# Kernel optimization log

Measured on AMD Instinct MI355X. Metric: run time of the kernel, lower is better.

Reference implementation:

```python
import jax, jax.numpy as jnp
import numpy as np

NUM_HEADS = 24
HEAD_DIM = 128
DIM = NUM_HEADS * HEAD_DIM  # 3072
EPS = 1e-6


def rms_norm(x, g):
    # x: [b, h, s, d], g: [d]
    var = jnp.mean(jnp.square(x.astype(jnp.float32)), axis=-1, keepdims=True)
    return (x.astype(jnp.float32) * jax.lax.rsqrt(var + EPS)).astype(x.dtype) * g


def apply_rope(x, cos, sin):
    # x: [b, h, s, d]; cos/sin: [s, d//2]; complex multiply on interleaved pairs
    b, h, s, d = x.shape
    xr = x.reshape(b, h, s, d // 2, 2)
    x0, x1 = xr[..., 0], xr[..., 1]
    c = cos[None, None, :, :]
    sn = sin[None, None, :, :]
    o0 = x0 * c - x1 * sn
    o1 = x0 * sn + x1 * c
    return jnp.stack([o0, o1], axis=-1).reshape(b, h, s, d)


def split_heads(x):
    # [b, s, h*d] -> [b, h, s, d]
    b, s, _ = x.shape
    return x.reshape(b, s, NUM_HEADS, HEAD_DIM).transpose(0, 2, 1, 3)


def setup_inputs() -> dict:
    key = jax.random.key(0)
    ks = jax.random.split(key, 16)
    b, s_img, s_txt = 1, 2048, 256
    image = jax.random.normal(ks[0], (b, s_img, DIM), jnp.float32)
    text = jax.random.normal(ks[1], (b, s_txt, DIM), jnp.float32)
    # rotary freqs: angles = pos * inv_freq
    half = HEAD_DIM // 2
    inv_freq = 1.0 / (10000.0 ** (np.arange(half, dtype=np.float32) / half))
    ang_i = np.arange(s_img, dtype=np.float32)[:, None] * inv_freq[None, :]
    ang_t = np.arange(s_txt, dtype=np.float32)[:, None] * inv_freq[None, :]
    img_cos, img_sin = jnp.cos(jnp.asarray(ang_i)), jnp.sin(jnp.asarray(ang_i))
    txt_cos, txt_sin = jnp.cos(jnp.asarray(ang_t)), jnp.sin(jnp.asarray(ang_t))
    sc = 1.0 / np.sqrt(DIM)
    Wqkv = jax.random.normal(ks[2], (DIM, 3 * DIM), jnp.float32) * sc
    bqkv = jnp.zeros((3 * DIM,), jnp.float32)
    Wadd = jax.random.normal(ks[3], (DIM, 3 * DIM), jnp.float32) * sc
    badd = jnp.zeros((3 * DIM,), jnp.float32)
    gq = jnp.ones((HEAD_DIM,), jnp.float32)
    gk = jnp.ones((HEAD_DIM,), jnp.float32)
    gaq = jnp.ones((HEAD_DIM,), jnp.float32)
    gak = jnp.ones((HEAD_DIM,), jnp.float32)
    Wout = jax.random.normal(ks[4], (DIM, DIM), jnp.float32) * sc
    bout = jnp.zeros((DIM,), jnp.float32)
    Waddout = jax.random.normal(ks[5], (DIM, DIM), jnp.float32) * sc
    baddout = jnp.zeros((DIM,), jnp.float32)
    return dict(image=image, text=text, img_cos=img_cos, img_sin=img_sin,
                txt_cos=txt_cos, txt_sin=txt_sin, Wqkv=Wqkv, bqkv=bqkv,
                Wadd=Wadd, badd=badd, gq=gq, gk=gk, gaq=gaq, gak=gak,
                Wout=Wout, bout=bout, Waddout=Waddout, baddout=baddout)


def reference(image, text, img_cos, img_sin, txt_cos, txt_sin,
              Wqkv, bqkv, Wadd, badd, gq, gk, gaq, gak,
              Wout, bout, Waddout, baddout):
    seq_txt = text.shape[1]
    img_qkv = image @ Wqkv + bqkv
    img_q, img_k, img_v = jnp.split(img_qkv, 3, axis=-1)
    txt_qkv = text @ Wadd + badd
    txt_q, txt_k, txt_v = jnp.split(txt_qkv, 3, axis=-1)

    img_q, img_k, img_v = split_heads(img_q), split_heads(img_k), split_heads(img_v)
    txt_q, txt_k, txt_v = split_heads(txt_q), split_heads(txt_k), split_heads(txt_v)

    img_q, img_k = rms_norm(img_q, gq), rms_norm(img_k, gk)
    txt_q, txt_k = rms_norm(txt_q, gaq), rms_norm(txt_k, gak)

    img_q = apply_rope(img_q, img_cos, img_sin)
    img_k = apply_rope(img_k, img_cos, img_sin)
    txt_q = apply_rope(txt_q, txt_cos, txt_sin)
    txt_k = apply_rope(txt_k, txt_cos, txt_sin)

    # joint attention: text tokens first, then image tokens
    q = jnp.concatenate([txt_q, img_q], axis=2)  # [b, h, S, d]
    k = jnp.concatenate([txt_k, img_k], axis=2)
    v = jnp.concatenate([txt_v, img_v], axis=2)

    scale = 1.0 / np.sqrt(HEAD_DIM)
    scores = jnp.einsum('bhqd,bhkd->bhqk', q, k) * scale
    probs = jax.nn.softmax(scores, axis=-1)
    attn = jnp.einsum('bhqk,bhkd->bhqd', probs, v)
    b, h, S, d = attn.shape
    attn = attn.transpose(0, 2, 1, 3).reshape(b, S, h * d)  # [b, S, dim]

    txt_out = attn[:, :seq_txt, :]
    img_out = attn[:, seq_txt:, :]
    img_out = img_out @ Wout + bout
    txt_out = txt_out @ Waddout + baddout
    return img_out, txt_out
```

## Files before the change

kernel.cpp:

```cpp
#include <hip/hip_runtime.h>

#define NH 24
#define HD 128
#define DM 3072
#define DM3 9216
#define STXT 256
#define SIMG 2048
#define SALL 2304

typedef __attribute__((ext_vector_type(8))) short bfrag;
typedef __attribute__((ext_vector_type(4))) float ffrag;

__device__ __forceinline__ unsigned short f2bf(float f) {
  unsigned int x = __builtin_bit_cast(unsigned int, f);
  x += 0x7fffu + ((x >> 16) & 1u);
  return (unsigned short)(x >> 16);
}

__global__ __launch_bounds__(256) void cast_kernel(const float* __restrict__ in,
                                                   unsigned short* __restrict__ out) {
  int i = blockIdx.x * 256 + threadIdx.x;
  float4 a = ((const float4*)in)[2 * i];
  float4 b = ((const float4*)in)[2 * i + 1];
  uint4 o;
  o.x = (unsigned)f2bf(a.x) | ((unsigned)f2bf(a.y) << 16);
  o.y = (unsigned)f2bf(a.z) | ((unsigned)f2bf(a.w) << 16);
  o.z = (unsigned)f2bf(b.x) | ((unsigned)f2bf(b.y) << 16);
  o.w = (unsigned)f2bf(b.z) | ((unsigned)f2bf(b.w) << 16);
  ((uint4*)out)[i] = o;
}

__global__ __launch_bounds__(256) void transpose_cast_kernel(const float* __restrict__ W,
                                                             unsigned short* __restrict__ Wt,
                                                             int K, int N) {
  __shared__ __align__(16) unsigned short tile[64 * 72];
  int k0 = blockIdx.y * 64, n0 = blockIdx.x * 64;
  int t = threadIdx.x;
  int rr = t >> 4, cc = (t & 15) * 4;
#pragma unroll
  for (int p = 0; p < 4; ++p) {
    int k = rr + p * 16;
    float4 v = *(const float4*)&W[(size_t)(k0 + k) * N + n0 + cc];
    tile[(cc + 0) * 72 + k] = f2bf(v.x);
    tile[(cc + 1) * 72 + k] = f2bf(v.y);
    tile[(cc + 2) * 72 + k] = f2bf(v.z);
    tile[(cc + 3) * 72 + k] = f2bf(v.w);
  }
  __syncthreads();
  int n = t >> 2, c = (t & 3) * 16;
  float4* dst = (float4*)&Wt[(size_t)(n0 + n) * K + k0 + c];
  dst[0] = *(float4*)&tile[n * 72 + c];
  dst[1] = *(float4*)&tile[n * 72 + c + 8];
}

__global__ __launch_bounds__(256) void gemm_bt(const unsigned short* __restrict__ A,
                                               const unsigned short* __restrict__ Bt,
                                               const float* __restrict__ bias,
                                               int M, int N, int K, int mode,
                                               float* __restrict__ outf,
                                               unsigned short* __restrict__ outb, int s_off) {
  __shared__ __align__(16) unsigned short As[128 * 40];
  __shared__ __align__(16) unsigned short Bs[128 * 40];
  const int tid = threadIdx.x;
  const int wave = tid >> 6, lane = tid & 63, quad = lane >> 4, l16 = lane & 15;
  const int wm = (wave >> 1) * 64, wn = (wave & 1) * 64;
  const size_t m0 = (size_t)blockIdx.y * 128, n0 = (size_t)blockIdx.x * 128;

  ffrag zf = {0.f, 0.f, 0.f, 0.f};
  ffrag acc[4][4];
#pragma unroll
  for (int i = 0; i < 4; ++i)
#pragma unroll
    for (int j = 0; j < 4; ++j) acc[i][j] = zf;

  const int sr = tid >> 2;
  const int sc = (tid & 3) * 8;
  const unsigned short* Ag = A + (m0 + sr) * K + sc;
  const unsigned short* Bg = Bt + (n0 + sr) * K + sc;

  for (int k0 = 0; k0 < K; k0 += 32) {
    __syncthreads();
    *(bfrag*)&As[sr * 40 + sc] = *(const bfrag*)&Ag[k0];
    *(bfrag*)&As[(sr + 64) * 40 + sc] = *(const bfrag*)&Ag[(size_t)64 * K + k0];
    *(bfrag*)&Bs[sr * 40 + sc] = *(const bfrag*)&Bg[k0];
    *(bfrag*)&Bs[(sr + 64) * 40 + sc] = *(const bfrag*)&Bg[(size_t)64 * K + k0];
    __syncthreads();
    bfrag af[4], bfv[4];
#pragma unroll
    for (int mt = 0; mt < 4; ++mt)
      af[mt] = *(const bfrag*)&As[(wm + mt * 16 + l16) * 40 + quad * 8];
#pragma unroll
    for (int nt = 0; nt < 4; ++nt)
      bfv[nt] = *(const bfrag*)&Bs[(wn + nt * 16 + l16) * 40 + quad * 8];
#pragma unroll
    for (int mt = 0; mt < 4; ++mt)
#pragma unroll
      for (int nt = 0; nt < 4; ++nt)
        acc[mt][nt] = __builtin_amdgcn_mfma_f32_16x16x32_bf16(af[mt], bfv[nt], acc[mt][nt], 0, 0, 0);
  }

  float bv[4];
#pragma unroll
  for (int nt = 0; nt < 4; ++nt) bv[nt] = bias[n0 + wn + nt * 16 + l16];

#pragma unroll
  for (int mt = 0; mt < 4; ++mt) {
#pragma unroll
    for (int nt = 0; nt < 4; ++nt) {
      int gn = (int)n0 + wn + nt * 16 + l16;
#pragma unroll
      for (int r = 0; r < 4; ++r) {
        float v = acc[mt][nt][r] + bv[nt];
        int gm = (int)m0 + wm + mt * 16 + quad * 4 + r;
        if (mode == 2) {
          outf[(size_t)gm * N + gn] = v;
        } else {
          int which = gn / DM;
          int rr2 = gn - which * DM;
          int head = rr2 >> 7, d = rr2 & 127;
          int s = s_off + gm;
          if (which < 2)
            outf[(((size_t)which * NH + head) * SALL + s) * HD + d] = v;
          else
            outb[((size_t)head * HD + d) * SALL + s] = f2bf(v);
        }
      }
    }
  }
}

__global__ __launch_bounds__(256) void norm_rope_kernel(
    const float* __restrict__ qkvf, const float* __restrict__ gq, const float* __restrict__ gk,
    const float* __restrict__ gaq, const float* __restrict__ gak,
    const float* __restrict__ img_cos, const float* __restrict__ img_sin,
    const float* __restrict__ txt_cos, const float* __restrict__ txt_sin,
    unsigned short* __restrict__ Qb, unsigned short* __restrict__ Kb) {
  int wave = threadIdx.x >> 6, lane = threadIdx.x & 63;
  int row = blockIdx.x * 4 + wave;
  int which = row / (NH * SALL);
  int rem = row - which * (NH * SALL);
  int s = rem % SALL;
  float2 v = *(const float2*)&qkvf[(size_t)row * HD + lane * 2];
  float ss = v.x * v.x + v.y * v.y;
#pragma unroll
  for (int m = 1; m < 64; m <<= 1) ss += __shfl_xor(ss, m);
  float rinv = rsqrtf(ss * (1.0f / 128.0f) + 1e-6f);
  bool is_txt = s < STXT;
  int pos = is_txt ? s : s - STXT;
  const float* g = (which == 0) ? (is_txt ? gaq : gq) : (is_txt ? gak : gk);
  const float* ct = is_txt ? txt_cos : img_cos;
  const float* st = is_txt ? txt_sin : img_sin;
  float c = ct[pos * 64 + lane], sn = st[pos * 64 + lane];
  float x0 = v.x * rinv * g[lane * 2];
  float x1 = v.y * rinv * g[lane * 2 + 1];
  float o0 = x0 * c - x1 * sn;
  float o1 = x0 * sn + x1 * c;
  unsigned short* out = (which == 0 ? Qb : Kb) + (size_t)rem * HD + lane * 2;
  *(unsigned int*)out = (unsigned)f2bf(o0) | ((unsigned)f2bf(o1) << 16);
}

__global__ __launch_bounds__(256) void flash_kernel(const unsigned short* __restrict__ Q,
                                                    const unsigned short* __restrict__ Kg,
                                                    const unsigned short* __restrict__ Vt,
                                                    unsigned short* __restrict__ attn) {
  __shared__ __align__(16) unsigned short Kl[64 * 136];
  __shared__ __align__(16) unsigned short Vl[128 * 72];
  __shared__ __align__(16) unsigned short Pl[4 * 16 * 72];
  const int h = blockIdx.y;
  const int qb = blockIdx.x * 64;
  const int tid = threadIdx.x;
  const int wave = tid >> 6, lane = tid & 63, quad = lane >> 4, l16 = lane & 15;

  const unsigned short* qrow = Q + ((size_t)h * SALL + qb + wave * 16 + l16) * HD;
  bfrag aq[4];
#pragma unroll
  for (int kk = 0; kk < 4; ++kk) aq[kk] = *(const bfrag*)&qrow[kk * 32 + quad * 8];

  ffrag zf = {0.f, 0.f, 0.f, 0.f};
  ffrag o[8];
#pragma unroll
  for (int i = 0; i < 8; ++i) o[i] = zf;
  float m_r[4] = {-__builtin_inff(), -__builtin_inff(), -__builtin_inff(), -__builtin_inff()};
  float l_r[4] = {0.f, 0.f, 0.f, 0.f};
  const float sc = 0.08838834764831845f * 1.4426950408889634f;

  for (int kb = 0; kb < SALL; kb += 64) {
    __syncthreads();
    {
      int r_ = tid >> 4, c_ = (tid & 15) * 8;
#pragma unroll
      for (int p = 0; p < 4; ++p)
        *(bfrag*)&Kl[(r_ + p * 16) * 136 + c_] =
            *(const bfrag*)&Kg[((size_t)h * SALL + kb + r_ + p * 16) * HD + c_];
      int dr = tid >> 3, dc = (tid & 7) * 8;
#pragma unroll
      for (int p = 0; p < 4; ++p)
        *(bfrag*)&Vl[(dr + p * 32) * 72 + dc] =
            *(const bfrag*)&Vt[((size_t)h * HD + dr + p * 32) * SALL + kb + dc];
    }
    __syncthreads();

    ffrag s_[4];
#pragma unroll
    for (int nt = 0; nt < 4; ++nt) s_[nt] = zf;
#pragma unroll
    for (int kk = 0; kk < 4; ++kk) {
#pragma unroll
      for (int nt = 0; nt < 4; ++nt) {
        bfrag kf = *(const bfrag*)&Kl[(nt * 16 + l16) * 136 + kk * 32 + quad * 8];
        s_[nt] = __builtin_amdgcn_mfma_f32_16x16x32_bf16(aq[kk], kf, s_[nt], 0, 0, 0);
      }
    }
#pragma unroll
    for (int nt = 0; nt < 4; ++nt)
#pragma unroll
      for (int r = 0; r < 4; ++r) s_[nt][r] *= sc;

    float alpha[4], rowsum[4];
#pragma unroll
    for (int r = 0; r < 4; ++r) {
      float mx = fmaxf(fmaxf(s_[0][r], s_[1][r]), fmaxf(s_[2][r], s_[3][r]));
#pragma unroll
      for (int msk = 1; msk < 16; msk <<= 1) mx = fmaxf(mx, __shfl_xor(mx, msk));
      float mnew = fmaxf(m_r[r], mx);
      alpha[r] = exp2f(m_r[r] - mnew);
      m_r[r] = mnew;
      float rs = 0.f;
#pragma unroll
      for (int nt = 0; nt < 4; ++nt) {
        float p = exp2f(s_[nt][r] - mnew);
        s_[nt][r] = p;
        rs += p;
      }
#pragma unroll
      for (int msk = 1; msk < 16; msk <<= 1) rs += __shfl_xor(rs, msk);
      rowsum[r] = rs;
      l_r[r] = l_r[r] * alpha[r] + rowsum[r];
    }
#pragma unroll
    for (int dt = 0; dt < 8; ++dt)
#pragma unroll
      for (int r = 0; r < 4; ++r) o[dt][r] *= alpha[r];
#pragma unroll
    for (int r = 0; r < 4; ++r)
#pragma unroll
      for (int nt = 0; nt < 4; ++nt)
        Pl[wave * 16 * 72 + (quad * 4 + r) * 72 + nt * 16 + l16] = f2bf(s_[nt][r]);
    __syncthreads();

    bfrag pf0 = *(const bfrag*)&Pl[wave * 16 * 72 + l16 * 72 + quad * 8];
    bfrag pf1 = *(const bfrag*)&Pl[wave * 16 * 72 + l16 * 72 + 32 + quad * 8];
#pragma unroll
    for (int dt = 0; dt < 8; ++dt) {
      bfrag vf0 = *(const bfrag*)&Vl[(dt * 16 + l16) * 72 + quad * 8];
      bfrag vf1 = *(const bfrag*)&Vl[(dt * 16 + l16) * 72 + 32 + quad * 8];
      o[dt] = __builtin_amdgcn_mfma_f32_16x16x32_bf16(pf0, vf0, o[dt], 0, 0, 0);
      o[dt] = __builtin_amdgcn_mfma_f32_16x16x32_bf16(pf1, vf1, o[dt], 0, 0, 0);
    }
  }

  float linv[4];
#pragma unroll
  for (int r = 0; r < 4; ++r) linv[r] = 1.0f / l_r[r];
#pragma unroll
  for (int dt = 0; dt < 8; ++dt) {
#pragma unroll
    for (int r = 0; r < 4; ++r) {
      int s = qb + wave * 16 + quad * 4 + r;
      attn[(size_t)s * DM + h * HD + dt * 16 + l16] = f2bf(o[dt][r] * linv[r]);
    }
  }
}

extern "C" void kernel_launch(void* const* d_in, const int* in_sizes, int n_in,
                              void* d_out, int out_size, void* d_ws, size_t ws_size,
                              hipStream_t stream) {
  const float* image = (const float*)d_in[0];
  const float* text = (const float*)d_in[1];
  const float* img_cos = (const float*)d_in[2];
  const float* img_sin = (const float*)d_in[3];
  const float* txt_cos = (const float*)d_in[4];
  const float* txt_sin = (const float*)d_in[5];
  const float* Wqkv = (const float*)d_in[6];
  const float* bqkv = (const float*)d_in[7];
  const float* Wadd = (const float*)d_in[8];
  const float* badd = (const float*)d_in[9];
  const float* gq = (const float*)d_in[10];
  const float* gk = (const float*)d_in[11];
  const float* gaq = (const float*)d_in[12];
  const float* gak = (const float*)d_in[13];
  const float* Wout = (const float*)d_in[14];
  const float* bout = (const float*)d_in[15];
  const float* Waddout = (const float*)d_in[16];
  const float* baddout = (const float*)d_in[17];

  char* ws = (char*)d_ws;
  size_t off = 0;
  unsigned short* img_bf = (unsigned short*)(ws + off); off += (size_t)SIMG * DM * 2;
  unsigned short* txt_bf = (unsigned short*)(ws + off); off += (size_t)STXT * DM * 2;
  unsigned short* attn = img_bf;
  unsigned short* Wqkv_t = (unsigned short*)(ws + off); off += (size_t)DM3 * DM * 2;
  unsigned short* Wadd_t = (unsigned short*)(ws + off); off += (size_t)DM3 * DM * 2;
  unsigned short* Wout_t = (unsigned short*)(ws + off); off += (size_t)DM * DM * 2;
  unsigned short* Waddout_t = (unsigned short*)(ws + off); off += (size_t)DM * DM * 2;
  float* qkvf = (float*)(ws + off); off += (size_t)2 * NH * SALL * HD * 4;
  unsigned short* Qb = (unsigned short*)(ws + off); off += (size_t)NH * SALL * HD * 2;
  unsigned short* Kb = (unsigned short*)(ws + off); off += (size_t)NH * SALL * HD * 2;
  unsigned short* Vtb = (unsigned short*)(ws + off); off += (size_t)NH * HD * SALL * 2;
  if (off > ws_size) return;

  cast_kernel<<<SIMG * DM / 2048, 256, 0, stream>>>(image, img_bf);
  cast_kernel<<<STXT * DM / 2048, 256, 0, stream>>>(text, txt_bf);
  transpose_cast_kernel<<<dim3(DM3 / 64, DM / 64), 256, 0, stream>>>(Wqkv, Wqkv_t, DM, DM3);
  transpose_cast_kernel<<<dim3(DM3 / 64, DM / 64), 256, 0, stream>>>(Wadd, Wadd_t, DM, DM3);
  transpose_cast_kernel<<<dim3(DM / 64, DM / 64), 256, 0, stream>>>(Wout, Wout_t, DM, DM);
  transpose_cast_kernel<<<dim3(DM / 64, DM / 64), 256, 0, stream>>>(Waddout, Waddout_t, DM, DM);

  gemm_bt<<<dim3(DM3 / 128, SIMG / 128), 256, 0, stream>>>(img_bf, Wqkv_t, bqkv, SIMG, DM3, DM,
                                                           0, qkvf, Vtb, STXT);
  gemm_bt<<<dim3(DM3 / 128, STXT / 128), 256, 0, stream>>>(txt_bf, Wadd_t, badd, STXT, DM3, DM,
                                                           0, qkvf, Vtb, 0);

  norm_rope_kernel<<<2 * NH * SALL / 4, 256, 0, stream>>>(qkvf, gq, gk, gaq, gak, img_cos,
                                                          img_sin, txt_cos, txt_sin, Qb, Kb);

  flash_kernel<<<dim3(SALL / 64, NH), 256, 0, stream>>>(Qb, Kb, Vtb, attn);

  gemm_bt<<<dim3(DM / 128, SIMG / 128), 256, 0, stream>>>(attn + (size_t)STXT * DM, Wout_t, bout,
                                                          SIMG, DM, DM, 2, (float*)d_out, nullptr, 0);
  gemm_bt<<<dim3(DM / 128, STXT / 128), 256, 0, stream>>>(attn, Waddout_t, baddout, STXT, DM, DM,
                                                          2, (float*)d_out + (size_t)SIMG * DM,
                                                          nullptr, 0);
}
```

Before: 1.046 ms.

## Use direct global-to-LDS loads with XOR-swizzled shared layouts in GEMM and flash attention

Replaces the register-staged global-to-shared copies in the GEMM and flash-attention kernels with `global_load_lds` 16-byte direct loads. The padded LDS rows give way to unpadded rows; in flash attention an XOR swizzle on K, V and P avoids bank conflicts. The block-wide barrier before reading the per-wave P tile is dropped, since each wave only touches its own region. This is meant to cut VGPR traffic, LDS footprint and a barrier per iteration. It relies on the compiler inserting correct waits for the async LDS writes and on intra-wave LDS ordering. The unswizzled GEMM layout may now see more bank conflicts.

```diff
diff --git a/kernel.cpp b/kernel.cpp
--- a/kernel.cpp
+++ b/kernel.cpp
@@ -15,6 +15,11 @@
   unsigned int x = __builtin_bit_cast(unsigned int, f);
   x += 0x7fffu + ((x >> 16) & 1u);
   return (unsigned short)(x >> 16);
+}
+
+__device__ __forceinline__ void gload16(void* lds, const void* g) {
+  __builtin_amdgcn_global_load_lds((const __attribute__((address_space(1))) unsigned int*)g,
+                                   (__attribute__((address_space(3))) unsigned int*)lds, 16, 0, 0);
 }
 
 __global__ __launch_bounds__(256) void cast_kernel(const float* __restrict__ in,
@@ -59,8 +64,8 @@
                                                int M, int N, int K, int mode,
                                                float* __restrict__ outf,
                                                unsigned short* __restrict__ outb, int s_off) {
-  __shared__ __align__(16) unsigned short As[128 * 40];
-  __shared__ __align__(16) unsigned short Bs[128 * 40];
+  __shared__ __align__(16) unsigned short As[128 * 32];
+  __shared__ __align__(16) unsigned short Bs[128 * 32];
   const int tid = threadIdx.x;
   const int wave = tid >> 6, lane = tid & 63, quad = lane >> 4, l16 = lane & 15;
   const int wm = (wave >> 1) * 64, wn = (wave & 1) * 64;
@@ -75,23 +80,27 @@
 
   const int sr = tid >> 2;
   const int sc = (tid & 3) * 8;
-  const unsigned short* Ag = A + (m0 + sr) * K + sc;
-  const unsigned short* Bg = Bt + (n0 + sr) * K + sc;
+  const unsigned short* Ag0 = A + (m0 + sr) * K + sc;
+  const unsigned short* Bg0 = Bt + (n0 + sr) * K + sc;
+  unsigned short* Ad0 = &As[sr * 32 + sc];
+  unsigned short* Ad1 = &As[(sr + 64) * 32 + sc];
+  unsigned short* Bd0 = &Bs[sr * 32 + sc];
+  unsigned short* Bd1 = &Bs[(sr + 64) * 32 + sc];
 
   for (int k0 = 0; k0 < K; k0 += 32) {
     __syncthreads();
-    *(bfrag*)&As[sr * 40 + sc] = *(const bfrag*)&Ag[k0];
-    *(bfrag*)&As[(sr + 64) * 40 + sc] = *(const bfrag*)&Ag[(size_t)64 * K + k0];
-    *(bfrag*)&Bs[sr * 40 + sc] = *(const bfrag*)&Bg[k0];
-    *(bfrag*)&Bs[(sr + 64) * 40 + sc] = *(const bfrag*)&Bg[(size_t)64 * K + k0];
+    gload16(Ad0, Ag0 + k0);
+    gload16(Ad1, Ag0 + (size_t)64 * K + k0);
+    gload16(Bd0, Bg0 + k0);
+    gload16(Bd1, Bg0 + (size_t)64 * K + k0);
     __syncthreads();
     bfrag af[4], bfv[4];
 #pragma unroll
     for (int mt = 0; mt < 4; ++mt)
-      af[mt] = *(const bfrag*)&As[(wm + mt * 16 + l16) * 40 + quad * 8];
+      af[mt] = *(const bfrag*)&As[(wm + mt * 16 + l16) * 32 + quad * 8];
 #pragma unroll
     for (int nt = 0; nt < 4; ++nt)
-      bfv[nt] = *(const bfrag*)&Bs[(wn + nt * 16 + l16) * 40 + quad * 8];
+      bfv[nt] = *(const bfrag*)&Bs[(wn + nt * 16 + l16) * 32 + quad * 8];
 #pragma unroll
     for (int mt = 0; mt < 4; ++mt)
 #pragma unroll
@@ -163,18 +172,22 @@
                                                     const unsigned short* __restrict__ Kg,
                                                     const unsigned short* __restrict__ Vt,
                                                     unsigned short* __restrict__ attn) {
-  __shared__ __align__(16) unsigned short Kl[64 * 136];
-  __shared__ __align__(16) unsigned short Vl[128 * 72];
-  __shared__ __align__(16) unsigned short Pl[4 * 16 * 72];
+  __shared__ __align__(16) unsigned short Kl[64 * 128];
+  __shared__ __align__(16) unsigned short Vl[128 * 64];
+  __shared__ __align__(16) unsigned short Pl[4 * 16 * 64];
   const int h = blockIdx.y;
   const int qb = blockIdx.x * 64;
   const int tid = threadIdx.x;
   const int wave = tid >> 6, lane = tid & 63, quad = lane >> 4, l16 = lane & 15;
+  const int l7 = l16 & 7;
 
   const unsigned short* qrow = Q + ((size_t)h * SALL + qb + wave * 16 + l16) * HD;
   bfrag aq[4];
 #pragma unroll
   for (int kk = 0; kk < 4; ++kk) aq[kk] = *(const bfrag*)&qrow[kk * 32 + quad * 8];
+
+  const unsigned short* Kh = Kg + (size_t)h * SALL * HD;
+  const unsigned short* Vh = Vt + (size_t)h * HD * SALL;
 
   ffrag zf = {0.f, 0.f, 0.f, 0.f};
   ffrag o[8];
@@ -186,17 +199,17 @@
 
   for (int kb = 0; kb < SALL; kb += 64) {
     __syncthreads();
-    {
-      int r_ = tid >> 4, c_ = (tid & 15) * 8;
-#pragma unroll
-      for (int p = 0; p < 4; ++p)
-        *(bfrag*)&Kl[(r_ + p * 16) * 136 + c_] =
-            *(const bfrag*)&Kg[((size_t)h * SALL + kb + r_ + p * 16) * HD + c_];
-      int dr = tid >> 3, dc = (tid & 7) * 8;
-#pragma unroll
-      for (int p = 0; p < 4; ++p)
-        *(bfrag*)&Vl[(dr + p * 32) * 72 + dc] =
-            *(const bfrag*)&Vt[((size_t)h * HD + dr + p * 32) * SALL + kb + dc];
+#pragma unroll
+    for (int p = 0; p < 4; ++p) {
+      int r = wave * 16 + p * 4 + quad;
+      int cs = l16 ^ (r & 7);
+      gload16(&Kl[r * 128 + l16 * 8], &Kh[(size_t)(kb + r) * HD + cs * 8]);
+    }
+#pragma unroll
+    for (int p = 0; p < 4; ++p) {
+      int r = wave * 32 + p * 8 + (lane >> 3);
+      int cs = (lane & 7) ^ (r & 7);
+      gload16(&Vl[r * 64 + (lane & 7) * 8], &Vh[(size_t)r * SALL + kb + cs * 8]);
     }
     __syncthreads();
 
@@ -207,7 +220,7 @@
     for (int kk = 0; kk < 4; ++kk) {
 #pragma unroll
       for (int nt = 0; nt < 4; ++nt) {
-        bfrag kf = *(const bfrag*)&Kl[(nt * 16 + l16) * 136 + kk * 32 + quad * 8];
+        bfrag kf = *(const bfrag*)&Kl[(nt * 16 + l16) * 128 + ((kk * 4 + quad) ^ l7) * 8];
         s_[nt] = __builtin_amdgcn_mfma_f32_16x16x32_bf16(aq[kk], kf, s_[nt], 0, 0, 0);
       }
     }
@@ -242,18 +255,19 @@
 #pragma unroll
       for (int r = 0; r < 4; ++r) o[dt][r] *= alpha[r];
 #pragma unroll
-    for (int r = 0; r < 4; ++r)
+    for (int r = 0; r < 4; ++r) {
+      int prow = quad * 4 + r;
 #pragma unroll
       for (int nt = 0; nt < 4; ++nt)
-        Pl[wave * 16 * 72 + (quad * 4 + r) * 72 + nt * 16 + l16] = f2bf(s_[nt][r]);
-    __syncthreads();
-
-    bfrag pf0 = *(const bfrag*)&Pl[wave * 16 * 72 + l16 * 72 + quad * 8];
-    bfrag pf1 = *(const bfrag*)&Pl[wave * 16 * 72 + l16 * 72 + 32 + quad * 8];
+        Pl[wave * 1024 + prow * 64 + ((nt * 16 + l16) ^ ((prow & 7) << 3))] = f2bf(s_[nt][r]);
+    }
+
+    bfrag pf0 = *(const bfrag*)&Pl[wave * 1024 + l16 * 64 + ((quad)     ^ l7) * 8];
+    bfrag pf1 = *(const bfrag*)&Pl[wave * 1024 + l16 * 64 + ((quad + 4) ^ l7) * 8];
 #pragma unroll
     for (int dt = 0; dt < 8; ++dt) {
-      bfrag vf0 = *(const bfrag*)&Vl[(dt * 16 + l16) * 72 + quad * 8];
-      bfrag vf1 = *(const bfrag*)&Vl[(dt * 16 + l16) * 72 + 32 + quad * 8];
+      bfrag vf0 = *(const bfrag*)&Vl[(dt * 16 + l16) * 64 + ((quad)     ^ l7) * 8];
+      bfrag vf1 = *(const bfrag*)&Vl[(dt * 16 + l16) * 64 + ((quad + 4) ^ l7) * 8];
       o[dt] = __builtin_amdgcn_mfma_f32_16x16x32_bf16(pf0, vf0, o[dt], 0, 0, 0);
       o[dt] = __builtin_amdgcn_mfma_f32_16x16x32_bf16(pf1, vf1, o[dt], 0, 0, 0);
     }
```

Measured after the change: 1.142 ms. 9.2% more time.
